# Performance work log

Hardware: AMD Instinct MI355X
Metric: run time of the kernel (lower is better)

Reference implementation:

```python
import jax, jax.numpy as jnp
import numpy as np

X_DIM = 362
N_EXPERTS = 3
HIDDEN = [1024, 2048, 2048, 1024]  # layer widths; final layer maps back to X_DIM


def _init_params(key):
    dims = [X_DIM] + HIDDEN + [X_DIM]
    params = {}
    for li in range(len(dims) - 1):
        fan_in = dims[li]
        kW, kb, key = jax.random.split(key, 3)
        bound = 1.0 / np.sqrt(fan_in)
        # stacked over experts: [E, in, out]
        params[f"W{li}"] = jax.random.uniform(kW, (N_EXPERTS, dims[li], dims[li + 1]), jnp.float32, -bound, bound)
        params[f"b{li}"] = jax.random.uniform(kb, (N_EXPERTS, dims[li + 1]), jnp.float32, -bound, bound)
    return params


def setup_inputs() -> dict:
    key = jax.random.key(0)
    kx, kn, ka, kp = jax.random.split(key, 4)
    B = 8192
    inp = {
        "batch_x": jax.random.normal(kx, (B, X_DIM), jnp.float32),
        "batch_next": jax.random.normal(kn, (B, X_DIM), jnp.float32),
        "batch_a": jax.random.randint(ka, (B,), 0, N_EXPERTS, jnp.int64),
    }
    inp.update(_init_params(kp))
    return inp


def _experts_forward(x, W0, b0, W1, b1, W2, b2, W3, b3, W4, b4):
    # Run every expert on the full batch (dense grouped GEMMs), then select.
    # h: [E, B, d]
    h = jax.nn.relu(jnp.einsum("bi,eio->ebo", x, W0) + b0[:, None, :])
    h = jax.nn.relu(jnp.einsum("ebi,eio->ebo", h, W1) + b1[:, None, :])
    h = jax.nn.relu(jnp.einsum("ebi,eio->ebo", h, W2) + b2[:, None, :])
    h = jax.nn.relu(jnp.einsum("ebi,eio->ebo", h, W3) + b3[:, None, :])
    return jnp.einsum("ebi,eio->ebo", h, W4) + b4[:, None, :]  # [E, B, X_DIM]


def reference(batch_x, batch_next, batch_a, W0, b0, W1, b1, W2, b2, W3, b3, W4, b4):
    preds = _experts_forward(batch_x, W0, b0, W1, b1, W2, b2, W3, b3, W4, b4)
    # route: pick each sample's prediction from its action's expert
    pred_next = preds[batch_a, jnp.arange(batch_x.shape[0])]  # [B, X_DIM]
    return jnp.mean((pred_next - batch_next) ** 2)
```

## Files before the change

kernel.cpp:

```cpp
#include <hip/hip_runtime.h>
#include <hip/hip_bf16.h>

#define B_SZ   8192
#define XD     362
#define NEXP   3
#define NTILES 70
#define MP     (NTILES*128)

typedef __bf16 bf16x8 __attribute__((ext_vector_type(8)));
typedef float  f32x4  __attribute__((ext_vector_type(4)));

__device__ __forceinline__ unsigned short f2bf(float f) {
    unsigned u = __float_as_uint(f);
    u += 0x7fffu + ((u >> 16) & 1u);
    return (unsigned short)(u >> 16);
}

__global__ __launch_bounds__(1024) void k_route(const int* __restrict__ a,
                                                int* __restrict__ hdr,
                                                int* __restrict__ row_of) {
    __shared__ int wpre[3][16];
    __shared__ int stot[3];
    int tid = threadIdx.x, lane = tid & 63, w = tid >> 6;
    int ev[8];
    int c0 = 0, c1 = 0, c2 = 0;
#pragma unroll
    for (int j = 0; j < 8; ++j) {
        int e = a[tid * 8 + j];
        ev[j] = e;
        c0 += (e == 0); c1 += (e == 1); c2 += (e == 2);
    }
    int i0 = c0, i1 = c1, i2 = c2;
#pragma unroll
    for (int off = 1; off < 64; off <<= 1) {
        int t0_ = __shfl_up(i0, off, 64);
        int t1_ = __shfl_up(i1, off, 64);
        int t2_ = __shfl_up(i2, off, 64);
        if (lane >= off) { i0 += t0_; i1 += t1_; i2 += t2_; }
    }
    if (lane == 63) { wpre[0][w] = i0; wpre[1][w] = i1; wpre[2][w] = i2; }
    __syncthreads();
    if (tid == 0) {
        int s0 = 0, s1 = 0, s2 = 0;
#pragma unroll
        for (int k = 0; k < 16; ++k) {
            int a0 = wpre[0][k], a1 = wpre[1][k], a2 = wpre[2][k];
            wpre[0][k] = s0; wpre[1][k] = s1; wpre[2][k] = s2;
            s0 += a0; s1 += a1; s2 += a2;
        }
        stot[0] = s0; stot[1] = s1; stot[2] = s2;
    }
    __syncthreads();
    int tot0 = stot[0], tot1 = stot[1], tot2 = stot[2];
    int t0 = ((tot0 + 255) >> 8) << 1;
    int t1 = ((tot1 + 255) >> 8) << 1;
    int t2 = ((tot2 + 255) >> 8) << 1;
    int seg0 = 0, seg1 = t0 * 128, seg2 = (t0 + t1) * 128;
    int nt = t0 + t1 + t2;
    int b0 = seg0 + wpre[0][w] + i0 - c0;
    int b1 = seg1 + wpre[1][w] + i1 - c1;
    int b2 = seg2 + wpre[2][w] + i2 - c2;
#pragma unroll
    for (int j = 0; j < 8; ++j) {
        int e = ev[j];
        int pos = (e == 0) ? b0++ : (e == 1) ? b1++ : b2++;
        row_of[pos] = tid * 8 + j;
    }
    if (tid == 0) {
        hdr[0] = tot0; hdr[1] = tot1; hdr[2] = tot2;
        hdr[6] = seg0; hdr[7] = seg1; hdr[8] = seg2;
        hdr[12] = nt;
        hdr[13] = nt / 2 - 1;
        hdr[16] = 0;
    }
    if (tid < NTILES)
        hdr[32 + tid] = (tid < t0) ? 0 : (tid < t0 + t1) ? 1 : (tid < nt) ? 2 : -1;
    for (int r = tid; r < MP; r += 1024) {
        int pad;
        if (r < seg1)           pad = (r - seg0) >= tot0;
        else if (r < seg2)      pad = (r - seg1) >= tot1;
        else if (r < nt * 128)  pad = (r - seg2) >= tot2;
        else                    pad = 1;
        if (pad) row_of[r] = -1;
    }
}

__global__ void k_gather(const float* __restrict__ x, const int* __restrict__ row_of,
                         unsigned short* __restrict__ xg) {
    int r = blockIdx.x;
    int c = threadIdx.x;
    int orig = row_of[r];
    float v = (orig >= 0 && c < XD) ? x[(size_t)orig * XD + c] : 0.f;
    xg[(size_t)r * 384 + c] = f2bf(v);
}

__device__ __forceinline__ void transpose_tile(const float* __restrict__ We,
                                               unsigned short* __restrict__ Wte,
                                               int K, int N, int Kp,
                                               int kb, int nb, int tx, int ty,
                                               float (*t)[33]) {
#pragma unroll
    for (int j = 0; j < 8; ++j) {
        int k = kb + ty + j * 8, n = nb + tx;
        t[ty + j * 8][tx] = (k < K && n < N) ? We[(size_t)k * N + n] : 0.f;
    }
    __syncthreads();
#pragma unroll
    for (int j = 0; j < 4; ++j) {
        int n = ty + j * 8;
        unsigned int lo = f2bf(t[2 * tx][n]);
        unsigned int hi = f2bf(t[2 * tx + 1][n]);
        *(unsigned int*)&Wte[(size_t)(nb + n) * Kp + kb + 2 * tx] = lo | (hi << 16);
    }
}

__global__ void k_transpose(const float* __restrict__ W, unsigned short* __restrict__ Wt,
                            int K, int N, int Kp, int Np) {
    __shared__ float t[64][33];
    int e  = blockIdx.z;
    int kb = blockIdx.x * 64, nb = blockIdx.y * 32;
    transpose_tile(W + (size_t)e * K * N, Wt + (size_t)e * Np * Kp,
                   K, N, Kp, kb, nb, threadIdx.x, threadIdx.y, t);
}

#define WT_OFF0 0
#define WT_OFF1 1179648u
#define WT_OFF2 7471104u
#define WT_OFF3 20054016u
#define WT_OFF4 26345472u
#define WT_TOTAL 27525120u

__global__ void k_transpose_all(const float* __restrict__ W0, const float* __restrict__ W1,
                                const float* __restrict__ W2, const float* __restrict__ W3,
                                const float* __restrict__ W4, unsigned short* __restrict__ Wt) {
    __shared__ float t[64][33];
    int ti = blockIdx.x, e = blockIdx.z;
    const float* W; int K, N, Kp, kt; unsigned off; int Np;
    if (ti < 192)       { W = W0; K = 362;  N = 1024; Kp = 384;  Np = 1024; kt = 6;  off = WT_OFF0; }
    else if (ti < 1216) { W = W1; K = 1024; N = 2048; Kp = 1024; Np = 2048; kt = 16; off = WT_OFF1; ti -= 192; }
    else if (ti < 3264) { W = W2; K = 2048; N = 2048; Kp = 2048; Np = 2048; kt = 32; off = WT_OFF2; ti -= 1216; }
    else if (ti < 4288) { W = W3; K = 2048; N = 1024; Kp = 2048; Np = 1024; kt = 32; off = WT_OFF3; ti -= 3264; }
    else                { W = W4; K = 1024; N = 362;  Kp = 1024; Np = 384;  kt = 16; off = WT_OFF4; ti -= 4288; }
    int kb = (ti % kt) * 64, nb = (ti / kt) * 32;
    transpose_tile(W + (size_t)e * K * N, Wt + off + (size_t)e * Np * Kp,
                   K, N, Kp, kb, nb, threadIdx.x, threadIdx.y, t);
}

template <int TM, int TN, int WAVES, bool FINAL, bool TAIL, bool SKIPLAST, int KSPLIT = 1>
__global__ __launch_bounds__(WAVES * 64) void k_gemm(
    const unsigned short* __restrict__ A, int lda,
    const unsigned short* __restrict__ Bt, int K, int Np,
    const float* __restrict__ bias, int nvalid,
    unsigned short* __restrict__ C, int ldc,
    const int* __restrict__ hdr,
    const float* __restrict__ nextv, const int* __restrict__ row_of,
    float* __restrict__ accum)
{
    __shared__ unsigned short As[2][TM * 64];
    __shared__ unsigned short Bs[2][TN * 64];
    __shared__ float red[WAVES];

    constexpr int WGN = TN / 64;
    constexpr int LA  = TM / (WAVES * 8);
    constexpr int LB  = TN / (WAVES * 8);

    int mt128;
    if constexpr (TAIL) {
        mt128 = hdr[13] * 2 + blockIdx.y;
    } else {
        if (SKIPLAST && (int)blockIdx.y >= hdr[13] && TM == 256) return;
        mt128 = blockIdx.y * (TM / 128);
    }
    int e = hdr[32 + mt128];
    if (e < 0) return;
    int row0 = mt128 * 128;
    int n0   = blockIdx.x * TN;

    int tid  = threadIdx.x;
    int wid  = tid >> 6, lane = tid & 63;
    int quad = lane >> 4, l15 = lane & 15;
    int sw   = l15 & 7;
    int wm = (wid / WGN) * 64, wn = (wid % WGN) * 64;

    const unsigned short* Ag = A  + (size_t)row0 * lda;
    const unsigned short* Bg = Bt + (size_t)e * Np * K + (size_t)n0 * K;
    const float* be = bias + (size_t)e * nvalid;

    int srow = lane >> 3;
    int scol = ((lane & 7) ^ srow) * 8;

    int kbeg = 0, kend = K;
    if constexpr (KSPLIT > 1) {
        int kh = K / KSPLIT;
        kbeg = blockIdx.z * kh;
        kend = kbeg + kh;
    }

    f32x4 acc[4][4];
#pragma unroll
    for (int i = 0; i < 4; ++i)
#pragma unroll
        for (int j = 0; j < 4; ++j)
            acc[i][j] = (f32x4){0.f, 0.f, 0.f, 0.f};

#define STAGE(K0, P)                                                              \
    {                                                                             \
        _Pragma("unroll")                                                         \
        for (int ii = 0; ii < LA; ++ii) {                                         \
            int rbase = wid * (TM / WAVES) + ii * 8;                              \
            const unsigned short* gp = Ag + (size_t)(rbase + srow) * lda + (K0) + scol; \
            __builtin_amdgcn_global_load_lds(                                     \
                (const __attribute__((address_space(1))) void*)gp,                \
                (__attribute__((address_space(3))) void*)(As[P] + rbase * 64), 16, 0, 0); \
        }                                                                         \
        _Pragma("unroll")                                                         \
        for (int ii = 0; ii < LB; ++ii) {                                         \
            int rbase = wid * (TN / WAVES) + ii * 8;                              \
            const unsigned short* gp = Bg + (size_t)(rbase + srow) * K + (K0) + scol;   \
            __builtin_amdgcn_global_load_lds(                                     \
                (const __attribute__((address_space(1))) void*)gp,                \
                (__attribute__((address_space(3))) void*)(Bs[P] + rbase * 64), 16, 0, 0); \
        }                                                                         \
    }

#define COMPUTE(P)                                                                \
    {                                                                             \
        _Pragma("unroll")                                                         \
        for (int kh2 = 0; kh2 < 2; ++kh2) {                                       \
            bf16x8 af[4], bfr[4];                                                 \
            _Pragma("unroll")                                                     \
            for (int f = 0; f < 4; ++f) {                                         \
                int row = wm + f * 16 + l15;                                      \
                af[f] = *(const bf16x8*)(As[P] + row * 64 + (((kh2 * 4 + quad) ^ sw) << 3)); \
            }                                                                     \
            _Pragma("unroll")                                                     \
            for (int f = 0; f < 4; ++f) {                                         \
                int row = wn + f * 16 + l15;                                      \
                bfr[f] = *(const bf16x8*)(Bs[P] + row * 64 + (((kh2 * 4 + quad) ^ sw) << 3)); \
            }                                                                     \
            _Pragma("unroll")                                                     \
            for (int fm = 0; fm < 4; ++fm)                                        \
                _Pragma("unroll")                                                 \
                for (int fn = 0; fn < 4; ++fn)                                    \
                    acc[fm][fn] = __builtin_amdgcn_mfma_f32_16x16x32_bf16(        \
                        af[fm], bfr[fn], acc[fm][fn], 0, 0, 0);                   \
        }                                                                         \
    }

    STAGE(kbeg, 0);
    __syncthreads();
    for (int k0 = kbeg; k0 < kend; k0 += 128) {
        if (k0 + 64 < kend) STAGE(k0 + 64, 1);
        COMPUTE(0);
        __syncthreads();
        if (k0 + 128 < kend) STAGE(k0 + 128, 0);
        COMPUTE(1);
        __syncthreads();
    }
#undef STAGE
#undef COMPUTE

    if constexpr (KSPLIT > 1) {
        float* P = accum + (size_t)blockIdx.z * 256 * Np;
#pragma unroll
        for (int fn = 0; fn < 4; ++fn) {
            int n = n0 + wn + fn * 16 + l15;
#pragma unroll
            for (int fm = 0; fm < 4; ++fm) {
#pragma unroll
                for (int i = 0; i < 4; ++i) {
                    int rl = blockIdx.y * 128 + wm + fm * 16 + quad * 4 + i;
                    P[(size_t)rl * Np + n] = acc[fm][fn][i];
                }
            }
        }
    } else if constexpr (!FINAL) {
#pragma unroll
        for (int fn = 0; fn < 4; ++fn) {
            int n = n0 + wn + fn * 16 + l15;
            float bv = be[n];
#pragma unroll
            for (int fm = 0; fm < 4; ++fm) {
#pragma unroll
                for (int i = 0; i < 4; ++i) {
                    int r = row0 + wm + fm * 16 + quad * 4 + i;
                    float v = acc[fm][fn][i] + bv;
                    v = v > 0.f ? v : 0.f;
                    C[(size_t)r * ldc + n] = f2bf(v);
                }
            }
        }
    } else {
        float local = 0.f;
#pragma unroll
        for (int fm = 0; fm < 4; ++fm) {
#pragma unroll
            for (int i = 0; i < 4; ++i) {
                int r = row0 + wm + fm * 16 + quad * 4 + i;
                int orig_r = row_of[r];
                if (orig_r >= 0) {
                    const float* nrow = nextv + (size_t)orig_r * XD;
#pragma unroll
                    for (int fn = 0; fn < 4; ++fn) {
                        int n = n0 + wn + fn * 16 + l15;
                        if (n < XD) {
                            float v = acc[fm][fn][i] + be[n];
                            float d = v - nrow[n];
                            local += d * d;
                        }
                    }
                }
            }
        }
        for (int off = 32; off > 0; off >>= 1)
            local += __shfl_down(local, off, 64);
        if (lane == 0) red[wid] = local;
        __syncthreads();
        if (tid == 0) {
            float s = 0.f;
#pragma unroll
            for (int w = 0; w < WAVES; ++w) s += red[w];
            atomicAdd(accum, s);
        }
    }
}

__global__ void k_tailc(const float* __restrict__ P, const float* __restrict__ bias,
                        int Np, int KS, unsigned short* __restrict__ C, int ldc,
                        const int* __restrict__ hdr) {
    int r = blockIdx.x;
    int e = hdr[32 + hdr[13] * 2];
    int row = hdr[13] * 256 + r;
    const float* be = bias + (size_t)e * Np;
    for (int n = threadIdx.x; n < Np; n += blockDim.x) {
        float s = 0.f;
        for (int z = 0; z < KS; ++z) s += P[((size_t)z * 256 + r) * Np + n];
        float v = s + be[n];
        v = v > 0.f ? v : 0.f;
        C[(size_t)row * ldc + n] = f2bf(v);
    }
}

__global__ void k_final(const int* hdr, float* out) {
    if (blockIdx.x == 0 && threadIdx.x == 0) {
        float s = ((const float*)hdr)[16];
        out[0] = s / (float)(B_SZ * XD);
    }
}

extern "C" void kernel_launch(void* const* d_in, const int* in_sizes, int n_in,
                              void* d_out, int out_size, void* d_ws, size_t ws_size,
                              hipStream_t stream) {
    const float* x     = (const float*)d_in[0];
    const float* nextv = (const float*)d_in[1];
    const int*   a     = (const int*)d_in[2];
    const float* W0 = (const float*)d_in[3],  *b0 = (const float*)d_in[4];
    const float* W1 = (const float*)d_in[5],  *b1 = (const float*)d_in[6];
    const float* W2 = (const float*)d_in[7],  *b2 = (const float*)d_in[8];
    const float* W3 = (const float*)d_in[9],  *b3 = (const float*)d_in[10];
    const float* W4 = (const float*)d_in[11], *b4 = (const float*)d_in[12];

    int* hdr    = (int*)d_ws;
    int* row_of = hdr + 128;
    unsigned short* xg = (unsigned short*)(row_of + MP);
    unsigned short* hA = xg + (size_t)MP * 384;
    unsigned short* hB = hA + (size_t)MP * 2048;
    unsigned short* Wt = hB + (size_t)MP * 2048;
    float* accum = (float*)(hdr + 16);

    size_t base = (size_t)(128 + MP) * 4 + (size_t)MP * 384 * 2 + (size_t)MP * 2048 * 2 * 2;
    const size_t PBYTES = (size_t)4 * 256 * 2048 * 4;
    bool merged = ws_size >= base + (size_t)WT_TOTAL * 2;
    float* Ppart = (float*)(Wt + WT_TOTAL);
    bool sk = merged && ws_size >= base + (size_t)WT_TOTAL * 2 + PBYTES;

    unsigned short *Wt0, *Wt1, *Wt2, *Wt3, *Wt4;
    if (merged) {
        Wt0 = Wt + WT_OFF0; Wt1 = Wt + WT_OFF1; Wt2 = Wt + WT_OFF2;
        Wt3 = Wt + WT_OFF3; Wt4 = Wt + WT_OFF4;
        k_transpose_all<<<dim3(4480, 1, 3), dim3(32, 8), 0, stream>>>(W0, W1, W2, W3, W4, Wt);
    } else {
        Wt0 = Wt1 = Wt2 = Wt3 = Wt4 = Wt;
    }

    k_route <<<1, 1024, 0, stream>>>(a, hdr, row_of);
    k_gather<<<MP, 384, 0, stream>>>(x, row_of, xg);

    if (!merged) k_transpose<<<dim3(6, 32, 3), dim3(32, 8), 0, stream>>>(W0, Wt0, XD, 1024, 384, 1024);
    k_gemm<128, 128, 4, false, false, false><<<dim3(8, NTILES), 256, 0, stream>>>(
        xg, 384, Wt0, 384, 1024, b0, 1024, hA, 1024, hdr, nullptr, nullptr, nullptr);

    if (!merged) k_transpose<<<dim3(16, 64, 3), dim3(32, 8), 0, stream>>>(W1, Wt1, 1024, 2048, 1024, 2048);
    k_gemm<256, 256, 16, false, false, true><<<dim3(8, NTILES / 2), 1024, 0, stream>>>(
        hA, 1024, Wt1, 1024, 2048, b1, 2048, hB, 2048, hdr, nullptr, nullptr, nullptr);
    if (sk) {
        k_gemm<128, 256, 8, false, true, false, 4><<<dim3(8, 2, 4), 512, 0, stream>>>(
            hA, 1024, Wt1, 1024, 2048, b1, 2048, hB, 2048, hdr, nullptr, nullptr, Ppart);
        k_tailc<<<256, 256, 0, stream>>>(Ppart, b1, 2048, 4, hB, 2048, hdr);
    } else {
        k_gemm<128, 256, 8, false, true, false><<<dim3(8, 2), 512, 0, stream>>>(
            hA, 1024, Wt1, 1024, 2048, b1, 2048, hB, 2048, hdr, nullptr, nullptr, nullptr);
    }

    if (!merged) k_transpose<<<dim3(32, 64, 3), dim3(32, 8), 0, stream>>>(W2, Wt2, 2048, 2048, 2048, 2048);
    k_gemm<256, 256, 16, false, false, true><<<dim3(8, NTILES / 2), 1024, 0, stream>>>(
        hB, 2048, Wt2, 2048, 2048, b2, 2048, hA, 2048, hdr, nullptr, nullptr, nullptr);
    if (sk) {
        k_gemm<128, 256, 8, false, true, false, 4><<<dim3(8, 2, 4), 512, 0, stream>>>(
            hB, 2048, Wt2, 2048, 2048, b2, 2048, hA, 2048, hdr, nullptr, nullptr, Ppart);
        k_tailc<<<256, 256, 0, stream>>>(Ppart, b2, 2048, 4, hA, 2048, hdr);
    } else {
        k_gemm<128, 256, 8, false, true, false><<<dim3(8, 2), 512, 0, stream>>>(
            hB, 2048, Wt2, 2048, 2048, b2, 2048, hA, 2048, hdr, nullptr, nullptr, nullptr);
    }

    if (!merged) k_transpose<<<dim3(32, 32, 3), dim3(32, 8), 0, stream>>>(W3, Wt3, 2048, 1024, 2048, 1024);
    k_gemm<256, 256, 16, false, false, true><<<dim3(4, NTILES / 2), 1024, 0, stream>>>(
        hA, 2048, Wt3, 2048, 1024, b3, 1024, hB, 1024, hdr, nullptr, nullptr, nullptr);
    if (sk) {
        k_gemm<128, 256, 8, false, true, false, 4><<<dim3(4, 2, 4), 512, 0, stream>>>(
            hA, 2048, Wt3, 2048, 1024, b3, 1024, hB, 1024, hdr, nullptr, nullptr, Ppart);
        k_tailc<<<256, 256, 0, stream>>>(Ppart, b3, 1024, 4, hB, 1024, hdr);
    } else {
        k_gemm<128, 256, 8, false, true, false><<<dim3(4, 2), 512, 0, stream>>>(
            hA, 2048, Wt3, 2048, 1024, b3, 1024, hB, 1024, hdr, nullptr, nullptr, nullptr);
    }

    if (!merged) k_transpose<<<dim3(16, 12, 3), dim3(32, 8), 0, stream>>>(W4, Wt4, 1024, XD, 1024, 384);
    k_gemm<128, 128, 4, true, false, false><<<dim3(3, NTILES), 256, 0, stream>>>(
        hB, 1024, Wt4, 1024, 384, b4, XD, nullptr, 0, hdr, nextv, row_of, accum);

    k_final<<<1, 64, 0, stream>>>(hdr, (float*)d_out);
}
```

Baseline: 487.5 us.

## Fuse tail-tile GEMM into main GEMM launch and vectorize gather

```diff
diff --git a/kernel.cpp b/kernel.cpp
--- a/kernel.cpp
+++ b/kernel.cpp
@@ -87,11 +87,19 @@
 
 __global__ void k_gather(const float* __restrict__ x, const int* __restrict__ row_of,
                          unsigned short* __restrict__ xg) {
-    int r = blockIdx.x;
-    int c = threadIdx.x;
-    int orig = row_of[r];
-    float v = (orig >= 0 && c < XD) ? x[(size_t)orig * XD + c] : 0.f;
-    xg[(size_t)r * 384 + c] = f2bf(v);
+    const int total = MP * 192;
+    unsigned* out = (unsigned*)xg;
+    for (int i = blockIdx.x * blockDim.x + threadIdx.x; i < total;
+         i += gridDim.x * blockDim.x) {
+        int r = i / 192, cu = i - r * 192, c = cu * 2;
+        int orig = row_of[r];
+        unsigned v = 0;
+        if (orig >= 0 && c < XD) {
+            float2 f = *(const float2*)&x[(size_t)orig * XD + c];
+            v = (unsigned)f2bf(f.x) | ((unsigned)f2bf(f.y) << 16);
+        }
+        out[(size_t)r * 192 + cu] = v;
+    }
 }
 
 __device__ __forceinline__ void transpose_tile(const float* __restrict__ We,
@@ -146,7 +154,7 @@
                    K, N, Kp, kb, nb, threadIdx.x, threadIdx.y, t);
 }
 
-template <int TM, int TN, int WAVES, bool FINAL, bool TAIL, bool SKIPLAST, int KSPLIT = 1>
+template <int TM, int TN, int WAVES, bool FINAL, int YMAIN, int KSPLIT>
 __global__ __launch_bounds__(WAVES * 64) void k_gemm(
     const unsigned short* __restrict__ A, int lda,
     const unsigned short* __restrict__ Bt, int K, int Np,
@@ -165,10 +173,15 @@
     constexpr int LB  = TN / (WAVES * 8);
 
     int mt128;
-    if constexpr (TAIL) {
-        mt128 = hdr[13] * 2 + blockIdx.y;
-    } else {
-        if (SKIPLAST && (int)blockIdx.y >= hdr[13] && TM == 256) return;
+    bool is_tail = false;
+    int zidx = 0;
+    if constexpr (YMAIN > 0) {
+        static_assert(TM == 256, "fused-tail mode requires TM==256");
+        int by = blockIdx.y;
+        if (by >= YMAIN) { is_tail = true; zidx = by - YMAIN; }
+        else if (by >= hdr[13]) return;
+        mt128 = is_tail ? hdr[13] * 2 : by * 2;
+    } else {
         mt128 = blockIdx.y * (TM / 128);
     }
     int e = hdr[32 + mt128];
@@ -190,9 +203,9 @@
     int scol = ((lane & 7) ^ srow) * 8;
 
     int kbeg = 0, kend = K;
-    if constexpr (KSPLIT > 1) {
+    if (is_tail && KSPLIT > 1) {
         int kh = K / KSPLIT;
-        kbeg = blockIdx.z * kh;
+        kbeg = zidx * kh;
         kend = kbeg + kh;
     }
 
@@ -260,21 +273,26 @@
 #undef STAGE
 #undef COMPUTE
 
-    if constexpr (KSPLIT > 1) {
-        float* P = accum + (size_t)blockIdx.z * 256 * Np;
-#pragma unroll
-        for (int fn = 0; fn < 4; ++fn) {
-            int n = n0 + wn + fn * 16 + l15;
-#pragma unroll
-            for (int fm = 0; fm < 4; ++fm) {
-#pragma unroll
-                for (int i = 0; i < 4; ++i) {
-                    int rl = blockIdx.y * 128 + wm + fm * 16 + quad * 4 + i;
-                    P[(size_t)rl * Np + n] = acc[fm][fn][i];
+    if constexpr (YMAIN > 0 && KSPLIT > 1) {
+        if (is_tail) {
+            float* P = accum + (size_t)zidx * 256 * Np;
+#pragma unroll
+            for (int fn = 0; fn < 4; ++fn) {
+                int n = n0 + wn + fn * 16 + l15;
+#pragma unroll
+                for (int fm = 0; fm < 4; ++fm) {
+#pragma unroll
+                    for (int i = 0; i < 4; ++i) {
+                        int rl = wm + fm * 16 + quad * 4 + i;
+                        P[(size_t)rl * Np + n] = acc[fm][fn][i];
+                    }
                 }
             }
-        }
-    } else if constexpr (!FINAL) {
+            return;
+        }
+    }
+
+    if constexpr (!FINAL) {
 #pragma unroll
         for (int fn = 0; fn < 4; ++fn) {
             int n = n0 + wn + fn * 16 + l15;
@@ -384,50 +402,44 @@
     }
 
     k_route <<<1, 1024, 0, stream>>>(a, hdr, row_of);
-    k_gather<<<MP, 384, 0, stream>>>(x, row_of, xg);
+    k_gather<<<1024, 256, 0, stream>>>(x, row_of, xg);
 
     if (!merged) k_transpose<<<dim3(6, 32, 3), dim3(32, 8), 0, stream>>>(W0, Wt0, XD, 1024, 384, 1024);
-    k_gemm<128, 128, 4, false, false, false><<<dim3(8, NTILES), 256, 0, stream>>>(
+    k_gemm<128, 128, 4, false, 0, 1><<<dim3(8, NTILES), 256, 0, stream>>>(
         xg, 384, Wt0, 384, 1024, b0, 1024, hA, 1024, hdr, nullptr, nullptr, nullptr);
 
     if (!merged) k_transpose<<<dim3(16, 64, 3), dim3(32, 8), 0, stream>>>(W1, Wt1, 1024, 2048, 1024, 2048);
-    k_gemm<256, 256, 16, false, false, true><<<dim3(8, NTILES / 2), 1024, 0, stream>>>(
-        hA, 1024, Wt1, 1024, 2048, b1, 2048, hB, 2048, hdr, nullptr, nullptr, nullptr);
     if (sk) {
-        k_gemm<128, 256, 8, false, true, false, 4><<<dim3(8, 2, 4), 512, 0, stream>>>(
+        k_gemm<256, 256, 16, false, NTILES / 2, 4><<<dim3(8, NTILES / 2 + 4), 1024, 0, stream>>>(
             hA, 1024, Wt1, 1024, 2048, b1, 2048, hB, 2048, hdr, nullptr, nullptr, Ppart);
         k_tailc<<<256, 256, 0, stream>>>(Ppart, b1, 2048, 4, hB, 2048, hdr);
     } else {
-        k_gemm<128, 256, 8, false, true, false><<<dim3(8, 2), 512, 0, stream>>>(
+        k_gemm<256, 256, 16, false, NTILES / 2, 1><<<dim3(8, NTILES / 2 + 1), 1024, 0, stream>>>(
             hA, 1024, Wt1, 1024, 2048, b1, 2048, hB, 2048, hdr, nullptr, nullptr, nullptr);
     }
 
     if (!merged) k_transpose<<<dim3(32, 64, 3), dim3(32, 8), 0, stream>>>(W2, Wt2, 2048, 2048, 2048, 2048);
-    k_gemm<256, 256, 16, false, false, true><<<dim3(8, NTILES / 2), 1024, 0, stream>>>(
-        hB, 2048, Wt2, 2048, 2048, b2, 2048, hA, 2048, hdr, nullptr, nullptr, nullptr);
     if (sk) {
-        k_gemm<128, 256, 8, false, true, false, 4><<<dim3(8, 2, 4), 512, 0, stream>>>(
+        k_gemm<256, 256, 16, false, NTILES / 2, 4><<<dim3(8, NTILES / 2 + 4), 1024, 0, stream>>>(
             hB, 2048, Wt2, 2048, 2048, b2, 2048, hA, 2048, hdr, nullptr, nullptr, Ppart);
         k_tailc<<<256, 256, 0, stream>>>(Ppart, b2, 2048, 4, hA, 2048, hdr);
     } else {
-        k_gemm<128, 256, 8, false, true, false><<<dim3(8, 2), 512, 0, stream>>>(
+        k_gemm<256, 256, 16, false, NTILES / 2, 1><<<dim3(8, NTILES / 2 + 1), 1024, 0, stream>>>(
             hB, 2048, Wt2, 2048, 2048, b2, 2048, hA, 2048, hdr, nullptr, nullptr, nullptr);
     }
 
     if (!merged) k_transpose<<<dim3(32, 32, 3), dim3(32, 8), 0, stream>>>(W3, Wt3, 2048, 1024, 2048, 1024);
-    k_gemm<256, 256, 16, false, false, true><<<dim3(4, NTILES / 2), 1024, 0, stream>>>(
-        hA, 2048, Wt3, 2048, 1024, b3, 1024, hB, 1024, hdr, nullptr, nullptr, nullptr);
     if (sk) {
-        k_gemm<128, 256, 8, false, true, false, 4><<<dim3(4, 2, 4), 512, 0, stream>>>(
+        k_gemm<256, 128, 8, false, NTILES / 2, 4><<<dim3(8, NTILES / 2 + 4), 512, 0, stream>>>(
             hA, 2048, Wt3, 2048, 1024, b3, 1024, hB, 1024, hdr, nullptr, nullptr, Ppart);
         k_tailc<<<256, 256, 0, stream>>>(Ppart, b3, 1024, 4, hB, 1024, hdr);
     } else {
-        k_gemm<128, 256, 8, false, true, false><<<dim3(4, 2), 512, 0, stream>>>(
+        k_gemm<256, 128, 8, false, NTILES / 2, 1><<<dim3(8, NTILES / 2 + 1), 512, 0, stream>>>(
             hA, 2048, Wt3, 2048, 1024, b3, 1024, hB, 1024, hdr, nullptr, nullptr, nullptr);
     }
 
     if (!merged) k_transpose<<<dim3(16, 12, 3), dim3(32, 8), 0, stream>>>(W4, Wt4, 1024, XD, 1024, 384);
-    k_gemm<128, 128, 4, true, false, false><<<dim3(3, NTILES), 256, 0, stream>>>(
+    k_gemm<128, 128, 4, true, 0, 1><<<dim3(3, NTILES), 256, 0, stream>>>(
         hB, 1024, Wt4, 1024, 384, b4, XD, nullptr, 0, hdr, nextv, row_of, accum);
 
     k_final<<<1, 64, 0, stream>>>(hdr, (float*)d_out);
```

Result: slower. 522.2 us (+7.1%).
